# Optimization experiments

Hardware: AMD Instinct MI355X
Metric: run time of the kernel (lower is better)

Reference implementation:

```python
import jax, jax.numpy as jnp
import numpy as np

HEAD_DIM = 128

def setup_inputs() -> dict:
    key = jax.random.key(0)
    k1, k2, k3 = jax.random.split(key, 3)
    B, Q, KV, H, D = 1, 2048, 2048, 32, HEAD_DIM
    q = jax.random.normal(k1, (B, Q, H, D), dtype=jnp.float32)
    k = jax.random.normal(k2, (B, KV, H, D), dtype=jnp.float32)
    v = jax.random.normal(k3, (B, KV, H, D), dtype=jnp.float32)
    # corm_mask row i is 1/(i+1), broadcast over kv_len (matches prepare())
    corm_mask = jnp.broadcast_to(1.0 / (jnp.arange(Q, dtype=jnp.float32) + 1.0)[:, None], (Q, KV))
    return {"q": q, "k": k, "v": v, "corm_mask": corm_mask}

def reference(q, k, v, corm_mask):
    B, Q, H, D = q.shape
    KV = k.shape[1]
    scale = 1.0 / jnp.sqrt(jnp.float32(D))
    # [B,H,Q,KV] attention scores
    scores = jnp.einsum('bqhd,bkhd->bhqk', q, k) * scale
    # causal mask: position i (query) attends to keys j <= i + (KV - Q)
    qi = jnp.arange(Q)[:, None]
    kj = jnp.arange(KV)[None, :]
    causal = kj <= qi + (KV - Q)  # [Q,KV]
    scores = jnp.where(causal[None, None], scores, -jnp.inf)
    probs = jax.nn.softmax(scores.astype(jnp.float32), axis=-1)
    out = jnp.einsum('bhqk,bkhd->bqhd', probs.astype(q.dtype), v)
    # per-key eviction mask: any query whose normalized prob >= threshold
    corm_score = jnp.any(probs >= corm_mask[None, None], axis=2)  # [B,H,KV]
    return out.reshape(B, Q, H, D), corm_score.reshape(B, H, KV)
```

## Files before the change

### kernel.cpp

```cpp
#include <hip/hip_runtime.h>
#include <math.h>


#define HN   32
#define DH   128
#define SEQ  2048
#define NBLK 32
#define KB   64
#define TILE_SHORTS 8192
#define SC2   0.1275174072417346f

typedef __attribute__((ext_vector_type(4))) float f4;
typedef __attribute__((ext_vector_type(8))) short s8;

__device__ __forceinline__ short f2bf(float x) {
  union { float f; unsigned u; } a; a.f = x;
  unsigned r = a.u + 0x7FFFu + ((a.u >> 16) & 1u);
  return (short)(r >> 16);
}
__device__ __forceinline__ float bf2f(short h) {
  union { unsigned u; float f; } a;
  a.u = ((unsigned)(unsigned short)h) << 16;
  return a.f;
}
__device__ __forceinline__ int swz(int row, int colShort, int Cshort) {
  int byte = (colShort * 2) ^ ((row & 7) << 4);
  return row * Cshort + (byte >> 1);
}
__device__ __forceinline__ float lanef(float v, int srcLane) {
  return __builtin_bit_cast(float,
      __builtin_amdgcn_ds_bpermute(srcLane * 4, __builtin_bit_cast(int, v)));
}

__global__ __launch_bounds__(256) void prep_qkv(
    const float* __restrict__ gQ, const float* __restrict__ gK,
    const float* __restrict__ gV, short* __restrict__ oQh,
    short* __restrict__ oQl, short* __restrict__ oKs, short* __restrict__ oVt,
    float* __restrict__ oC)
{
  __shared__ short Vs[64][136];
  const int blk = blockIdx.x, h = blockIdx.y, tid = threadIdx.x;
  const size_t toff = ((size_t)h * NBLK + blk) * TILE_SHORTS;

  if (tid < 64) oC[h * SEQ + blk * 64 + tid] = 0.f;

#pragma unroll
  for (int i = 0; i < 4; ++i) {
    int f = tid + 256 * i;
    int n = f >> 8, dt = (f >> 6) & 3, l4 = (f >> 4) & 3, l15 = f & 15;
    int r = n * 16 + l15, c0 = dt * 32 + l4 * 8;
    size_t rowoff = ((size_t)(blk * 64 + r) * HN + h) * DH + c0;
    {
      f4 a = *(const f4*)(gQ + rowoff), b = *(const f4*)(gQ + rowoff + 4);
      s8 oh, ol;
#pragma unroll
      for (int e = 0; e < 4; ++e) {
        float sa = a[e] * SC2, sb = b[e] * SC2;
        short hi = f2bf(sa); oh[e] = hi; ol[e] = f2bf(sa - bf2f(hi));
        short h2 = f2bf(sb); oh[4+e] = h2; ol[4+e] = f2bf(sb - bf2f(h2));
      }
      *(s8*)&oQh[toff + (size_t)f * 8] = oh;
      *(s8*)&oQl[toff + (size_t)f * 8] = ol;
    }
    {
      f4 a = *(const f4*)(gK + rowoff), b = *(const f4*)(gK + rowoff + 4);
      s8 o;
#pragma unroll
      for (int e = 0; e < 4; ++e) { o[e] = f2bf(a[e]); o[4+e] = f2bf(b[e]); }
      *(s8*)&oKs[toff + (size_t)f * 8] = o;
    }
    {
      f4 a = *(const f4*)(gV + rowoff), b = *(const f4*)(gV + rowoff + 4);
      s8 o;
#pragma unroll
      for (int e = 0; e < 4; ++e) { o[e] = f2bf(a[e]); o[4+e] = f2bf(b[e]); }
      *(s8*)&Vs[r][c0] = o;
    }
  }
  __syncthreads();
#pragma unroll
  for (int i = 0; i < 4; ++i) {
    int f = tid + 256 * i;
    int ds = f >> 7, hf = (f >> 6) & 1, l4 = (f >> 4) & 3, l15 = f & 15;
    int d = ds * 16 + l15, k0 = hf * 32 + l4 * 8;
    s8 o;
#pragma unroll
    for (int j = 0; j < 8; ++j) o[j] = Vs[k0 + j][d];
    *(s8*)&oVt[toff + (size_t)f * 8] = o;
  }
}

__global__ __launch_bounds__(128) void flash_fwd(
    const short* __restrict__ gQh, const short* __restrict__ gKs,
    const short* __restrict__ gVt, float* __restrict__ gO,
    float* __restrict__ gT)
{
  __shared__ __align__(16) char smem[16896];
  f4*    obuf = (f4*)smem;
  float* lbuf = (float*)(smem + 16384);

  const int id = blockIdx.x;
  const int xcd = id & 7, jj = id >> 3;
  const int h = xcd + 8 * (jj >> 6);
  const int b32 = 63 - (jj & 63);
  const int tid = threadIdx.x;
  const int wv = tid >> 6, ln = tid & 63, l15 = ln & 15, l4 = ln >> 4;
  const int q0 = b32 * 32;
  const int btile = q0 >> 6;
  const int ntile = btile + 1;
  const int h1 = (ntile + 1) >> 1;
  const int tstart = wv ? h1 : 0, tend = wv ? ntile : h1;
  const size_t hbase = (size_t)h * NBLK * TILE_SHORTS;
  const int abase = (ln & 48) + 4 * l4;

  const short* qtile = gQh + hbase + (size_t)btile * TILE_SHORTS;
  s8 qf[2][4];
#pragma unroll
  for (int g = 0; g < 2; ++g)
#pragma unroll
    for (int dt = 0; dt < 4; ++dt)
      qf[g][dt] = *(const s8*)&qtile[(size_t)(((((b32 & 1) * 2 + g) * 4 + dt) * 64 + ln)) * 8];

  f4 oacc[2][8];
#pragma unroll
  for (int g = 0; g < 2; ++g)
#pragma unroll
    for (int i = 0; i < 8; ++i) { oacc[g][i][0]=0.f; oacc[g][i][1]=0.f; oacc[g][i][2]=0.f; oacc[g][i][3]=0.f; }
  float l1[2] = {0.f, 0.f};

  const short* kp = gKs + hbase + (size_t)tstart * TILE_SHORTS;
  const short* vp = gVt + hbase + (size_t)tstart * TILE_SHORTS;

  for (int t = tstart; t < tend; ++t) {
    s8 kf[4][4];
#pragma unroll
    for (int n = 0; n < 4; ++n)
#pragma unroll
      for (int dt = 0; dt < 4; ++dt)
        kf[n][dt] = *(const s8*)&kp[(size_t)(((n * 4 + dt) * 64 + ln)) * 8];
    s8 vb[8][2];
#pragma unroll
    for (int ds = 0; ds < 8; ++ds)
#pragma unroll
      for (int hf = 0; hf < 2; ++hf)
        vb[ds][hf] = *(const s8*)&vp[(size_t)(((ds * 2 + hf) * 64 + ln)) * 8];

    f4 sacc[2][4];
#pragma unroll
    for (int g = 0; g < 2; ++g)
#pragma unroll
      for (int n = 0; n < 4; ++n) { sacc[g][n][0]=0.f; sacc[g][n][1]=0.f; sacc[g][n][2]=0.f; sacc[g][n][3]=0.f; }
    __builtin_amdgcn_s_setprio(1);
#pragma unroll
    for (int n = 0; n < 4; ++n)
#pragma unroll
      for (int dt = 0; dt < 4; ++dt) {
        sacc[0][n] = __builtin_amdgcn_mfma_f32_16x16x32_bf16(kf[n][dt], qf[0][dt], sacc[0][n], 0, 0, 0);
        sacc[1][n] = __builtin_amdgcn_mfma_f32_16x16x32_bf16(kf[n][dt], qf[1][dt], sacc[1][n], 0, 0, 0);
      }
    __builtin_amdgcn_s_setprio(0);

    if (t == btile) {
#pragma unroll
      for (int g = 0; g < 2; ++g) {
        const int qg = q0 + g * 16 + l15;
#pragma unroll
        for (int n = 0; n < 4; ++n)
#pragma unroll
          for (int j = 0; j < 4; ++j) {
            int kv = t * 64 + n * 16 + 4 * l4 + j;
            if (kv > qg) sacc[g][n][j] = -INFINITY;
          }
      }
    }

#pragma unroll
    for (int g = 0; g < 2; ++g) {
      float s0 = 0.f;
#pragma unroll
      for (int n = 0; n < 4; ++n) {
#pragma unroll
        for (int j = 0; j < 4; ++j) sacc[g][n][j] = __builtin_amdgcn_exp2f(sacc[g][n][j]);
        s0 += (sacc[g][n][0] + sacc[g][n][1]) + (sacc[g][n][2] + sacc[g][n][3]);
      }
      l1[g] += s0;
    }

#pragma unroll
    for (int g = 0; g < 2; ++g) {
      short* pw = (short*)(smem + wv * 4096 + g * 2048);
#pragma unroll
      for (int n = 0; n < 4; ++n) {
        unsigned lo, hi;
        asm("v_cvt_pk_bf16_f32 %0, %1, %2" : "=v"(lo) : "v"(sacc[g][n][0]), "v"(sacc[g][n][1]));
        asm("v_cvt_pk_bf16_f32 %0, %1, %2" : "=v"(hi) : "v"(sacc[g][n][2]), "v"(sacc[g][n][3]));
        uint2 w; w.x = lo; w.y = hi;
        *(uint2*)&pw[swz(l15, n * 16 + 4 * l4, KB)] = w;
      }
    }

    const short* pw0 = (const short*)(smem + wv * 4096);
    const short* pw1 = (const short*)(smem + wv * 4096 + 2048);
    s8 pa00 = *(const s8*)&pw0[swz(l15, l4 * 8, KB)];
    s8 pa01 = *(const s8*)&pw0[swz(l15, 32 + l4 * 8, KB)];
    s8 pa10 = *(const s8*)&pw1[swz(l15, l4 * 8, KB)];
    s8 pa11 = *(const s8*)&pw1[swz(l15, 32 + l4 * 8, KB)];
    __builtin_amdgcn_s_setprio(1);
#pragma unroll
    for (int ds = 0; ds < 8; ++ds) {
      oacc[0][ds] = __builtin_amdgcn_mfma_f32_16x16x32_bf16(pa00, vb[ds][0], oacc[0][ds], 0, 0, 0);
      oacc[1][ds] = __builtin_amdgcn_mfma_f32_16x16x32_bf16(pa10, vb[ds][0], oacc[1][ds], 0, 0, 0);
      oacc[0][ds] = __builtin_amdgcn_mfma_f32_16x16x32_bf16(pa01, vb[ds][1], oacc[0][ds], 0, 0, 0);
      oacc[1][ds] = __builtin_amdgcn_mfma_f32_16x16x32_bf16(pa11, vb[ds][1], oacc[1][ds], 0, 0, 0);
    }
    __builtin_amdgcn_s_setprio(0);
    kp += TILE_SHORTS; vp += TILE_SHORTS;
  }

  __syncthreads();
  if (wv == 1) {
#pragma unroll
    for (int g = 0; g < 2; ++g) {
#pragma unroll
      for (int ds = 0; ds < 8; ++ds)
        obuf[(g * 8 + ds) * 64 + ln] = oacc[g][ds];
      lbuf[g * 64 + ln] = l1[g];
    }
  }
  __syncthreads();
  if (wv == 1) return;

#pragma unroll
  for (int g = 0; g < 2; ++g) {
    l1[g] += lbuf[g * 64 + ln];
#pragma unroll
    for (int ds = 0; ds < 8; ++ds) {
      f4 ob = obuf[(g * 8 + ds) * 64 + ln];
#pragma unroll
      for (int j = 0; j < 4; ++j) oacc[g][ds][j] += ob[j];
    }
  }

#pragma unroll
  for (int g = 0; g < 2; ++g) {
    l1[g] += __shfl_xor(l1[g], 16);
    l1[g] += __shfl_xor(l1[g], 32);
  }
#pragma unroll
  for (int g = 0; g < 2; ++g) {
    float linv = 1.0f / l1[g];
    float lj[4];
#pragma unroll
    for (int j = 0; j < 4; ++j) lj[j] = lanef(linv, abase + j);
#pragma unroll
    for (int j = 0; j < 4; ++j) {
      int qg = q0 + g * 16 + 4 * l4 + j;
      float* orow = gO + ((size_t)qg * HN + h) * DH;
#pragma unroll
      for (int ds = 0; ds < 8; ++ds)
        orow[ds * 16 + l15] = oacc[g][ds][j] * lj[j];
    }
    if (l4 == 0) {
      int qg = q0 + g * 16 + l15;
      gT[h * SEQ + qg] = log2f(l1[g]) - log2f((float)(qg + 1));
    }
  }
}

__global__ __launch_bounds__(128) void corm_fwd(
    const float* __restrict__ gK, const short* __restrict__ gQh,
    const short* __restrict__ gQl, const float* __restrict__ gT,
    float* __restrict__ gC)
{
  __shared__ float Tt[512];

  const int id = blockIdx.x;
  const int xcd = id & 7, r = id >> 3;
  const int h = xcd + 8 * (r / 80);
  const int s = r % 80;
  int m, c;
  if (s < 32)      { m = s >> 2;             c = s & 3;  }
  else if (s < 56) { int k = s - 32; m = 8  + k / 3;  c = k % 3; }
  else if (s < 72) { int k = s - 56; m = 16 + (k >> 1); c = k & 1; }
  else             { m = 24 + (s - 72);      c = 0; }
  const int kvb = m * 64;
  const int tb = m + 8 * c;
  const int te = (tb + 8 < NBLK) ? tb + 8 : NBLK;

  const int tid = threadIdx.x;
  const int wv = tid >> 6, ln = tid & 63, l15 = ln & 15, l4 = ln >> 4;
  const int kvw = kvb + wv * 32;

  for (int i = tid; i < (te - tb) * 64; i += 128)
    Tt[i] = gT[h * SEQ + tb * 64 + i];

  s8 khi[2][4], klo[2][4];
#pragma unroll
  for (int g = 0; g < 2; ++g) {
    const float* krow = gK + ((size_t)(kvw + g * 16 + l15) * HN + h) * DH;
#pragma unroll
    for (int dt = 0; dt < 4; ++dt) {
      f4 a = *(const f4*)(krow + dt * 32 + l4 * 8);
      f4 bb = *(const f4*)(krow + dt * 32 + l4 * 8 + 4);
#pragma unroll
      for (int e = 0; e < 4; ++e) {
        short hi = f2bf(a[e]); khi[g][dt][e] = hi; klo[g][dt][e] = f2bf(a[e] - bf2f(hi));
        short h2 = f2bf(bb[e]); khi[g][dt][4+e] = h2; klo[g][dt][4+e] = f2bf(bb[e] - bf2f(h2));
      }
    }
  }
  __syncthreads();

  const size_t hbase = (size_t)h * NBLK * TILE_SHORTS;
  int fired[2][4] = {{0,0,0,0},{0,0,0,0}};

  for (int t = tb; t < te; ++t) {
    const short* qht = gQh + hbase + (size_t)t * TILE_SHORTS;
    const short* qlt = gQl + hbase + (size_t)t * TILE_SHORTS;
    float Tq4[4];
#pragma unroll
    for (int n = 0; n < 4; ++n)
      Tq4[n] = Tt[(t - tb) * 64 + n * 16 + l15];

#pragma unroll
    for (int n = 0; n < 4; ++n) {
      s8 qhb[4], qlb[4];
#pragma unroll
      for (int dt = 0; dt < 4; ++dt) {
        qhb[dt] = *(const s8*)&qht[(size_t)(((n * 4 + dt) * 64 + ln)) * 8];
        qlb[dt] = *(const s8*)&qlt[(size_t)(((n * 4 + dt) * 64 + ln)) * 8];
      }
      f4 acc0, acc1;
      acc0[0]=0.f; acc0[1]=0.f; acc0[2]=0.f; acc0[3]=0.f;
      acc1 = acc0;
      __builtin_amdgcn_s_setprio(1);
#pragma unroll
      for (int dt = 0; dt < 4; ++dt) {
        acc0 = __builtin_amdgcn_mfma_f32_16x16x32_bf16(khi[0][dt], qhb[dt], acc0, 0, 0, 0);
        acc0 = __builtin_amdgcn_mfma_f32_16x16x32_bf16(khi[0][dt], qlb[dt], acc0, 0, 0, 0);
        acc0 = __builtin_amdgcn_mfma_f32_16x16x32_bf16(klo[0][dt], qhb[dt], acc0, 0, 0, 0);
        acc1 = __builtin_amdgcn_mfma_f32_16x16x32_bf16(khi[1][dt], qhb[dt], acc1, 0, 0, 0);
        acc1 = __builtin_amdgcn_mfma_f32_16x16x32_bf16(khi[1][dt], qlb[dt], acc1, 0, 0, 0);
        acc1 = __builtin_amdgcn_mfma_f32_16x16x32_bf16(klo[1][dt], qhb[dt], acc1, 0, 0, 0);
      }
      __builtin_amdgcn_s_setprio(0);
      int qg = t * 64 + n * 16 + l15;
      float Tq = Tq4[n];
#pragma unroll
      for (int j = 0; j < 4; ++j) {
        int kvr0 = kvw + 4 * l4 + j;
        if (qg >= kvr0 && acc0[j] >= Tq) fired[0][j] = 1;
        int kvr1 = kvw + 16 + 4 * l4 + j;
        if (qg >= kvr1 && acc1[j] >= Tq) fired[1][j] = 1;
      }
    }
  }

#pragma unroll
  for (int g = 0; g < 2; ++g)
#pragma unroll
    for (int j = 0; j < 4; ++j) {
      fired[g][j] |= __shfl_xor(fired[g][j], 1, 16);
      fired[g][j] |= __shfl_xor(fired[g][j], 2, 16);
      fired[g][j] |= __shfl_xor(fired[g][j], 4, 16);
      fired[g][j] |= __shfl_xor(fired[g][j], 8, 16);
    }
  if (l15 == 0) {
#pragma unroll
    for (int g = 0; g < 2; ++g)
#pragma unroll
      for (int j = 0; j < 4; ++j)
        if (fired[g][j])
          gC[h * SEQ + kvw + g * 16 + 4 * l4 + j] = 1.0f;
  }
}

extern "C" void kernel_launch(void* const* d_in, const int* in_sizes, int n_in,
                              void* d_out, int out_size, void* d_ws, size_t ws_size,
                              hipStream_t stream) {
  const float* q = (const float*)d_in[0];
  const float* k = (const float*)d_in[1];
  const float* v = (const float*)d_in[2];
  float* out  = (float*)d_out;
  float* corm = out + (size_t)SEQ * HN * DH;

  const size_t ARR = (size_t)HN * NBLK * TILE_SHORTS;
  short* Qh = (short*)d_ws;
  short* Ql = Qh + ARR;
  short* Ks = Ql + ARR;
  short* Vt = Ks + ARR;
  float* T  = (float*)(Vt + ARR);

  prep_qkv<<<dim3(NBLK, HN), dim3(256), 0, stream>>>(q, k, v, Qh, Ql, Ks, Vt, corm);
  flash_fwd<<<dim3(2048), dim3(128), 0, stream>>>(Qh, Ks, Vt, out, T);
  corm_fwd<<<dim3(2560), dim3(128), 0, stream>>>(k, Qh, Ql, T, corm);
}
```

Baseline: 152.4 us.

## Share K/V and Q tiles across four waves via direct global-to-LDS staging

flash_fwd now runs 4 waves per block, each owning 32 query rows, and cooperatively stages each K and V tile into LDS with global_load_lds, replacing per-wave global register loads and the two-wave split-KV merge. corm_fwd similarly moves to 256-thread blocks covering 128 keys and stages Qhi/Qlo tiles in LDS shared by all waves. This aims to cut redundant global/L2 traffic, at the cost of block-wide barriers with no double buffering and idle waves on causal-masked tiles.

```diff
diff --git a/kernel.cpp b/kernel.cpp
--- a/kernel.cpp
+++ b/kernel.cpp
@@ -13,6 +13,9 @@
 typedef __attribute__((ext_vector_type(4))) float f4;
 typedef __attribute__((ext_vector_type(8))) short s8;
 
+typedef __attribute__((address_space(3))) unsigned lds_u32;
+typedef const __attribute__((address_space(1))) unsigned glob_u32;
+
 __device__ __forceinline__ short f2bf(float x) {
   union { float f; unsigned u; } a; a.f = x;
   unsigned r = a.u + 0x7FFFu + ((a.u >> 16) & 1u);
@@ -30,6 +33,14 @@
 __device__ __forceinline__ float lanef(float v, int srcLane) {
   return __builtin_bit_cast(float,
       __builtin_amdgcn_ds_bpermute(srcLane * 4, __builtin_bit_cast(int, v)));
+}
+__device__ __forceinline__ void stage_tile(const char* gsrc, char* ldst,
+                                           int wv, int ln) {
+#pragma unroll
+  for (int i = 0; i < 4; ++i)
+    __builtin_amdgcn_global_load_lds(
+        (glob_u32*)(gsrc + wv * 4096 + i * 1024 + ln * 16),
+        (lds_u32*)(ldst + wv * 4096 + i * 1024), 16, 0, 0);
 }
 
 __global__ __launch_bounds__(256) void prep_qkv(
@@ -90,36 +101,34 @@
   }
 }
 
-__global__ __launch_bounds__(128) void flash_fwd(
+__global__ __launch_bounds__(256) void flash_fwd(
     const short* __restrict__ gQh, const short* __restrict__ gKs,
     const short* __restrict__ gVt, float* __restrict__ gO,
     float* __restrict__ gT)
 {
-  __shared__ __align__(16) char smem[16896];
-  f4*    obuf = (f4*)smem;
-  float* lbuf = (float*)(smem + 16384);
+  __shared__ short Kl[TILE_SHORTS];
+  __shared__ short Vl[TILE_SHORTS];
+  __shared__ short Ps[4][2][1024];
 
   const int id = blockIdx.x;
   const int xcd = id & 7, jj = id >> 3;
-  const int h = xcd + 8 * (jj >> 6);
-  const int b32 = 63 - (jj & 63);
+  const int h = xcd + 8 * (jj >> 4);
+  const int b = 15 - (jj & 15);
   const int tid = threadIdx.x;
   const int wv = tid >> 6, ln = tid & 63, l15 = ln & 15, l4 = ln >> 4;
-  const int q0 = b32 * 32;
-  const int btile = q0 >> 6;
-  const int ntile = btile + 1;
-  const int h1 = (ntile + 1) >> 1;
-  const int tstart = wv ? h1 : 0, tend = wv ? ntile : h1;
+  const int q0 = b * 128 + wv * 32;
+  const int dtile = q0 >> 6;
   const size_t hbase = (size_t)h * NBLK * TILE_SHORTS;
+  const int ntile = 2 * b + 2;
   const int abase = (ln & 48) + 4 * l4;
 
-  const short* qtile = gQh + hbase + (size_t)btile * TILE_SHORTS;
+  const short* qtile = gQh + hbase + (size_t)(2 * b + (wv >> 1)) * TILE_SHORTS;
   s8 qf[2][4];
 #pragma unroll
   for (int g = 0; g < 2; ++g)
 #pragma unroll
     for (int dt = 0; dt < 4; ++dt)
-      qf[g][dt] = *(const s8*)&qtile[(size_t)(((((b32 & 1) * 2 + g) * 4 + dt) * 64 + ln)) * 8];
+      qf[g][dt] = *(const s8*)&qtile[(size_t)(((((wv & 1) * 2 + g) * 4 + dt) * 64 + ln)) * 8];
 
   f4 oacc[2][8];
 #pragma unroll
@@ -128,117 +137,96 @@
     for (int i = 0; i < 8; ++i) { oacc[g][i][0]=0.f; oacc[g][i][1]=0.f; oacc[g][i][2]=0.f; oacc[g][i][3]=0.f; }
   float l1[2] = {0.f, 0.f};
 
-  const short* kp = gKs + hbase + (size_t)tstart * TILE_SHORTS;
-  const short* vp = gVt + hbase + (size_t)tstart * TILE_SHORTS;
-
-  for (int t = tstart; t < tend; ++t) {
-    s8 kf[4][4];
-#pragma unroll
-    for (int n = 0; n < 4; ++n)
-#pragma unroll
-      for (int dt = 0; dt < 4; ++dt)
-        kf[n][dt] = *(const s8*)&kp[(size_t)(((n * 4 + dt) * 64 + ln)) * 8];
-    s8 vb[8][2];
-#pragma unroll
-    for (int ds = 0; ds < 8; ++ds)
-#pragma unroll
-      for (int hf = 0; hf < 2; ++hf)
-        vb[ds][hf] = *(const s8*)&vp[(size_t)(((ds * 2 + hf) * 64 + ln)) * 8];
-
-    f4 sacc[2][4];
-#pragma unroll
-    for (int g = 0; g < 2; ++g)
-#pragma unroll
-      for (int n = 0; n < 4; ++n) { sacc[g][n][0]=0.f; sacc[g][n][1]=0.f; sacc[g][n][2]=0.f; sacc[g][n][3]=0.f; }
-    __builtin_amdgcn_s_setprio(1);
-#pragma unroll
-    for (int n = 0; n < 4; ++n)
-#pragma unroll
-      for (int dt = 0; dt < 4; ++dt) {
-        sacc[0][n] = __builtin_amdgcn_mfma_f32_16x16x32_bf16(kf[n][dt], qf[0][dt], sacc[0][n], 0, 0, 0);
-        sacc[1][n] = __builtin_amdgcn_mfma_f32_16x16x32_bf16(kf[n][dt], qf[1][dt], sacc[1][n], 0, 0, 0);
-      }
-    __builtin_amdgcn_s_setprio(0);
-
-    if (t == btile) {
+  const char* kp = (const char*)(gKs + hbase);
+  const char* vp = (const char*)(gVt + hbase);
+
+  for (int t = 0; t < ntile; ++t) {
+    stage_tile(kp, (char*)Kl, wv, ln);
+    stage_tile(vp, (char*)Vl, wv, ln);
+    asm volatile("s_waitcnt vmcnt(0)" ::: "memory");
+    __builtin_amdgcn_s_barrier();
+    __builtin_amdgcn_sched_barrier(0);
+
+    if (t * 64 <= q0 + 31) {
+      f4 sacc[2][4];
+#pragma unroll
+      for (int g = 0; g < 2; ++g)
+#pragma unroll
+        for (int n = 0; n < 4; ++n) { sacc[g][n][0]=0.f; sacc[g][n][1]=0.f; sacc[g][n][2]=0.f; sacc[g][n][3]=0.f; }
+      __builtin_amdgcn_s_setprio(1);
+#pragma unroll
+      for (int n = 0; n < 4; ++n) {
+        s8 kf[4];
+#pragma unroll
+        for (int dt = 0; dt < 4; ++dt)
+          kf[dt] = *(const s8*)&Kl[((n * 4 + dt) * 64 + ln) * 8];
+#pragma unroll
+        for (int dt = 0; dt < 4; ++dt) {
+          sacc[0][n] = __builtin_amdgcn_mfma_f32_16x16x32_bf16(kf[dt], qf[0][dt], sacc[0][n], 0, 0, 0);
+          sacc[1][n] = __builtin_amdgcn_mfma_f32_16x16x32_bf16(kf[dt], qf[1][dt], sacc[1][n], 0, 0, 0);
+        }
+      }
+      __builtin_amdgcn_s_setprio(0);
+
+      if (t == dtile) {
+#pragma unroll
+        for (int g = 0; g < 2; ++g) {
+          const int qg = q0 + g * 16 + l15;
+#pragma unroll
+          for (int n = 0; n < 4; ++n)
+#pragma unroll
+            for (int j = 0; j < 4; ++j) {
+              int kv = t * 64 + n * 16 + 4 * l4 + j;
+              if (kv > qg) sacc[g][n][j] = -INFINITY;
+            }
+        }
+      }
+
 #pragma unroll
       for (int g = 0; g < 2; ++g) {
-        const int qg = q0 + g * 16 + l15;
-#pragma unroll
-        for (int n = 0; n < 4; ++n)
-#pragma unroll
-          for (int j = 0; j < 4; ++j) {
-            int kv = t * 64 + n * 16 + 4 * l4 + j;
-            if (kv > qg) sacc[g][n][j] = -INFINITY;
-          }
-      }
-    }
-
-#pragma unroll
-    for (int g = 0; g < 2; ++g) {
-      float s0 = 0.f;
-#pragma unroll
-      for (int n = 0; n < 4; ++n) {
-#pragma unroll
-        for (int j = 0; j < 4; ++j) sacc[g][n][j] = __builtin_amdgcn_exp2f(sacc[g][n][j]);
-        s0 += (sacc[g][n][0] + sacc[g][n][1]) + (sacc[g][n][2] + sacc[g][n][3]);
-      }
-      l1[g] += s0;
-    }
-
-#pragma unroll
-    for (int g = 0; g < 2; ++g) {
-      short* pw = (short*)(smem + wv * 4096 + g * 2048);
-#pragma unroll
-      for (int n = 0; n < 4; ++n) {
-        unsigned lo, hi;
-        asm("v_cvt_pk_bf16_f32 %0, %1, %2" : "=v"(lo) : "v"(sacc[g][n][0]), "v"(sacc[g][n][1]));
-        asm("v_cvt_pk_bf16_f32 %0, %1, %2" : "=v"(hi) : "v"(sacc[g][n][2]), "v"(sacc[g][n][3]));
-        uint2 w; w.x = lo; w.y = hi;
-        *(uint2*)&pw[swz(l15, n * 16 + 4 * l4, KB)] = w;
-      }
-    }
-
-    const short* pw0 = (const short*)(smem + wv * 4096);
-    const short* pw1 = (const short*)(smem + wv * 4096 + 2048);
-    s8 pa00 = *(const s8*)&pw0[swz(l15, l4 * 8, KB)];
-    s8 pa01 = *(const s8*)&pw0[swz(l15, 32 + l4 * 8, KB)];
-    s8 pa10 = *(const s8*)&pw1[swz(l15, l4 * 8, KB)];
-    s8 pa11 = *(const s8*)&pw1[swz(l15, 32 + l4 * 8, KB)];
-    __builtin_amdgcn_s_setprio(1);
-#pragma unroll
-    for (int ds = 0; ds < 8; ++ds) {
-      oacc[0][ds] = __builtin_amdgcn_mfma_f32_16x16x32_bf16(pa00, vb[ds][0], oacc[0][ds], 0, 0, 0);
-      oacc[1][ds] = __builtin_amdgcn_mfma_f32_16x16x32_bf16(pa10, vb[ds][0], oacc[1][ds], 0, 0, 0);
-      oacc[0][ds] = __builtin_amdgcn_mfma_f32_16x16x32_bf16(pa01, vb[ds][1], oacc[0][ds], 0, 0, 0);
-      oacc[1][ds] = __builtin_amdgcn_mfma_f32_16x16x32_bf16(pa11, vb[ds][1], oacc[1][ds], 0, 0, 0);
-    }
-    __builtin_amdgcn_s_setprio(0);
-    kp += TILE_SHORTS; vp += TILE_SHORTS;
-  }
-
-  __syncthreads();
-  if (wv == 1) {
-#pragma unroll
-    for (int g = 0; g < 2; ++g) {
-#pragma unroll
-      for (int ds = 0; ds < 8; ++ds)
-        obuf[(g * 8 + ds) * 64 + ln] = oacc[g][ds];
-      lbuf[g * 64 + ln] = l1[g];
-    }
-  }
-  __syncthreads();
-  if (wv == 1) return;
-
-#pragma unroll
-  for (int g = 0; g < 2; ++g) {
-    l1[g] += lbuf[g * 64 + ln];
-#pragma unroll
-    for (int ds = 0; ds < 8; ++ds) {
-      f4 ob = obuf[(g * 8 + ds) * 64 + ln];
-#pragma unroll
-      for (int j = 0; j < 4; ++j) oacc[g][ds][j] += ob[j];
-    }
+        float s0 = 0.f;
+#pragma unroll
+        for (int n = 0; n < 4; ++n) {
+#pragma unroll
+          for (int j = 0; j < 4; ++j) sacc[g][n][j] = __builtin_amdgcn_exp2f(sacc[g][n][j]);
+          s0 += (sacc[g][n][0] + sacc[g][n][1]) + (sacc[g][n][2] + sacc[g][n][3]);
+        }
+        l1[g] += s0;
+      }
+
+#pragma unroll
+      for (int g = 0; g < 2; ++g) {
+        short* pw = &Ps[wv][g][0];
+#pragma unroll
+        for (int n = 0; n < 4; ++n) {
+          unsigned lo, hi;
+          asm("v_cvt_pk_bf16_f32 %0, %1, %2" : "=v"(lo) : "v"(sacc[g][n][0]), "v"(sacc[g][n][1]));
+          asm("v_cvt_pk_bf16_f32 %0, %1, %2" : "=v"(hi) : "v"(sacc[g][n][2]), "v"(sacc[g][n][3]));
+          uint2 w; w.x = lo; w.y = hi;
+          *(uint2*)&pw[swz(l15, n * 16 + 4 * l4, KB)] = w;
+        }
+      }
+
+      s8 pa00 = *(const s8*)&Ps[wv][0][swz(l15, l4 * 8, KB)];
+      s8 pa01 = *(const s8*)&Ps[wv][0][swz(l15, 32 + l4 * 8, KB)];
+      s8 pa10 = *(const s8*)&Ps[wv][1][swz(l15, l4 * 8, KB)];
+      s8 pa11 = *(const s8*)&Ps[wv][1][swz(l15, 32 + l4 * 8, KB)];
+      __builtin_amdgcn_s_setprio(1);
+#pragma unroll
+      for (int ds = 0; ds < 8; ++ds) {
+        s8 vb0 = *(const s8*)&Vl[((ds * 2 + 0) * 64 + ln) * 8];
+        s8 vb1 = *(const s8*)&Vl[((ds * 2 + 1) * 64 + ln) * 8];
+        oacc[0][ds] = __builtin_amdgcn_mfma_f32_16x16x32_bf16(pa00, vb0, oacc[0][ds], 0, 0, 0);
+        oacc[1][ds] = __builtin_amdgcn_mfma_f32_16x16x32_bf16(pa10, vb0, oacc[1][ds], 0, 0, 0);
+        oacc[0][ds] = __builtin_amdgcn_mfma_f32_16x16x32_bf16(pa01, vb1, oacc[0][ds], 0, 0, 0);
+        oacc[1][ds] = __builtin_amdgcn_mfma_f32_16x16x32_bf16(pa11, vb1, oacc[1][ds], 0, 0, 0);
+      }
+      __builtin_amdgcn_s_setprio(0);
+    }
+    asm volatile("s_waitcnt lgkmcnt(0)" ::: "memory");
+    __builtin_amdgcn_s_barrier();
+    __builtin_amdgcn_sched_barrier(0);
+    kp += TILE_SHORTS * 2; vp += TILE_SHORTS * 2;
   }
 
 #pragma unroll
@@ -267,31 +255,26 @@
   }
 }
 
-__global__ __launch_bounds__(128) void corm_fwd(
+__global__ __launch_bounds__(256) void corm_fwd(
     const float* __restrict__ gK, const short* __restrict__ gQh,
     const short* __restrict__ gQl, const float* __restrict__ gT,
     float* __restrict__ gC)
 {
+  __shared__ short Qhl[TILE_SHORTS];
+  __shared__ short Qll[TILE_SHORTS];
   __shared__ float Tt[512];
 
-  const int id = blockIdx.x;
-  const int xcd = id & 7, r = id >> 3;
-  const int h = xcd + 8 * (r / 80);
-  const int s = r % 80;
-  int m, c;
-  if (s < 32)      { m = s >> 2;             c = s & 3;  }
-  else if (s < 56) { int k = s - 32; m = 8  + k / 3;  c = k % 3; }
-  else if (s < 72) { int k = s - 56; m = 16 + (k >> 1); c = k & 1; }
-  else             { m = 24 + (s - 72);      c = 0; }
-  const int kvb = m * 64;
-  const int tb = m + 8 * c;
+  const int h = blockIdx.x, m = blockIdx.y, c = blockIdx.z;
+  const int tb = 2 * m + 8 * c;
+  if (tb >= NBLK) return;
   const int te = (tb + 8 < NBLK) ? tb + 8 : NBLK;
+  const int kvb = m * 128;
 
   const int tid = threadIdx.x;
   const int wv = tid >> 6, ln = tid & 63, l15 = ln & 15, l4 = ln >> 4;
   const int kvw = kvb + wv * 32;
 
-  for (int i = tid; i < (te - tb) * 64; i += 128)
+  for (int i = tid; i < (te - tb) * 64; i += 256)
     Tt[i] = gT[h * SEQ + tb * 64 + i];
 
   s8 khi[2][4], klo[2][4];
@@ -312,48 +295,60 @@
   __syncthreads();
 
   const size_t hbase = (size_t)h * NBLK * TILE_SHORTS;
+  const char* qhp = (const char*)(gQh + hbase + (size_t)tb * TILE_SHORTS);
+  const char* qlp = (const char*)(gQl + hbase + (size_t)tb * TILE_SHORTS);
   int fired[2][4] = {{0,0,0,0},{0,0,0,0}};
 
   for (int t = tb; t < te; ++t) {
-    const short* qht = gQh + hbase + (size_t)t * TILE_SHORTS;
-    const short* qlt = gQl + hbase + (size_t)t * TILE_SHORTS;
-    float Tq4[4];
-#pragma unroll
-    for (int n = 0; n < 4; ++n)
-      Tq4[n] = Tt[(t - tb) * 64 + n * 16 + l15];
-
-#pragma unroll
-    for (int n = 0; n < 4; ++n) {
-      s8 qhb[4], qlb[4];
-#pragma unroll
-      for (int dt = 0; dt < 4; ++dt) {
-        qhb[dt] = *(const s8*)&qht[(size_t)(((n * 4 + dt) * 64 + ln)) * 8];
-        qlb[dt] = *(const s8*)&qlt[(size_t)(((n * 4 + dt) * 64 + ln)) * 8];
-      }
-      f4 acc0, acc1;
-      acc0[0]=0.f; acc0[1]=0.f; acc0[2]=0.f; acc0[3]=0.f;
-      acc1 = acc0;
+    stage_tile(qhp, (char*)Qhl, wv, ln);
+    stage_tile(qlp, (char*)Qll, wv, ln);
+    asm volatile("s_waitcnt vmcnt(0)" ::: "memory");
+    __builtin_amdgcn_s_barrier();
+    __builtin_amdgcn_sched_barrier(0);
+
+    if (kvw <= t * 64 + 63) {
+      float Tq4[4];
+#pragma unroll
+      for (int n = 0; n < 4; ++n)
+        Tq4[n] = Tt[(t - tb) * 64 + n * 16 + l15];
+
       __builtin_amdgcn_s_setprio(1);
 #pragma unroll
-      for (int dt = 0; dt < 4; ++dt) {
-        acc0 = __builtin_amdgcn_mfma_f32_16x16x32_bf16(khi[0][dt], qhb[dt], acc0, 0, 0, 0);
-        acc0 = __builtin_amdgcn_mfma_f32_16x16x32_bf16(khi[0][dt], qlb[dt], acc0, 0, 0, 0);
-        acc0 = __builtin_amdgcn_mfma_f32_16x16x32_bf16(klo[0][dt], qhb[dt], acc0, 0, 0, 0);
-        acc1 = __builtin_amdgcn_mfma_f32_16x16x32_bf16(khi[1][dt], qhb[dt], acc1, 0, 0, 0);
-        acc1 = __builtin_amdgcn_mfma_f32_16x16x32_bf16(khi[1][dt], qlb[dt], acc1, 0, 0, 0);
-        acc1 = __builtin_amdgcn_mfma_f32_16x16x32_bf16(klo[1][dt], qhb[dt], acc1, 0, 0, 0);
+      for (int n = 0; n < 4; ++n) {
+        s8 qhb[4], qlb[4];
+#pragma unroll
+        for (int dt = 0; dt < 4; ++dt) {
+          qhb[dt] = *(const s8*)&Qhl[((n * 4 + dt) * 64 + ln) * 8];
+          qlb[dt] = *(const s8*)&Qll[((n * 4 + dt) * 64 + ln) * 8];
+        }
+        f4 acc0, acc1;
+        acc0[0]=0.f; acc0[1]=0.f; acc0[2]=0.f; acc0[3]=0.f;
+        acc1 = acc0;
+#pragma unroll
+        for (int dt = 0; dt < 4; ++dt) {
+          acc0 = __builtin_amdgcn_mfma_f32_16x16x32_bf16(khi[0][dt], qhb[dt], acc0, 0, 0, 0);
+          acc0 = __builtin_amdgcn_mfma_f32_16x16x32_bf16(khi[0][dt], qlb[dt], acc0, 0, 0, 0);
+          acc0 = __builtin_amdgcn_mfma_f32_16x16x32_bf16(klo[0][dt], qhb[dt], acc0, 0, 0, 0);
+          acc1 = __builtin_amdgcn_mfma_f32_16x16x32_bf16(khi[1][dt], qhb[dt], acc1, 0, 0, 0);
+          acc1 = __builtin_amdgcn_mfma_f32_16x16x32_bf16(khi[1][dt], qlb[dt], acc1, 0, 0, 0);
+          acc1 = __builtin_amdgcn_mfma_f32_16x16x32_bf16(klo[1][dt], qhb[dt], acc1, 0, 0, 0);
+        }
+        int qg = t * 64 + n * 16 + l15;
+        float Tq = Tq4[n];
+#pragma unroll
+        for (int j = 0; j < 4; ++j) {
+          int kvr0 = kvw + 4 * l4 + j;
+          if (qg >= kvr0 && acc0[j] >= Tq) fired[0][j] = 1;
+          int kvr1 = kvw + 16 + 4 * l4 + j;
+          if (qg >= kvr1 && acc1[j] >= Tq) fired[1][j] = 1;
+        }
       }
       __builtin_amdgcn_s_setprio(0);
-      int qg = t * 64 + n * 16 + l15;
-      float Tq = Tq4[n];
-#pragma unroll
-      for (int j = 0; j < 4; ++j) {
-        int kvr0 = kvw + 4 * l4 + j;
-        if (qg >= kvr0 && acc0[j] >= Tq) fired[0][j] = 1;
-        int kvr1 = kvw + 16 + 4 * l4 + j;
-        if (qg >= kvr1 && acc1[j] >= Tq) fired[1][j] = 1;
-      }
-    }
+    }
+    asm volatile("s_waitcnt lgkmcnt(0)" ::: "memory");
+    __builtin_amdgcn_s_barrier();
+    __builtin_amdgcn_sched_barrier(0);
+    qhp += TILE_SHORTS * 2; qlp += TILE_SHORTS * 2;
   }
 
 #pragma unroll
@@ -392,6 +387,6 @@
   float* T  = (float*)(Vt + ARR);
 
   prep_qkv<<<dim3(NBLK, HN), dim3(256), 0, stream>>>(q, k, v, Qh, Ql, Ks, Vt, corm);
-  flash_fwd<<<dim3(2048), dim3(128), 0, stream>>>(Qh, Ks, Vt, out, T);
-  corm_fwd<<<dim3(2560), dim3(128), 0, stream>>>(k, Qh, Ql, T, corm);
-}
+  flash_fwd<<<dim3(512), dim3(256), 0, stream>>>(Qh, Ks, Vt, out, T);
+  corm_fwd<<<dim3(32, 16, 4), dim3(256), 0, stream>>>(k, Qh, Ql, T, corm);
+}
```

Measured after the change: 165.3 us. +8.5%, slower.
